# Kernel tuning notes

Measured on AMD Instinct MI355X. Metric: run time of the kernel, lower is better.

Reference implementation:

```python
import jax, jax.numpy as jnp
import numpy as np

HEADS = 16
DIM = 1024
HEAD_DIM = DIM // HEADS


def setup_inputs() -> dict:
    key = jax.random.key(0)
    k1, k2 = jax.random.split(key)
    images = jax.random.normal(k1, (2, 2048, DIM), dtype=jnp.float32)
    # torch nn.Linear(dim, 3*dim, bias=False): y = x @ W.T, W: [3*dim, dim].
    # Store as [dim, 3*dim] for direct x @ W_qkv.
    W_qkv = jax.random.normal(k2, (DIM, 3 * DIM), dtype=jnp.float32) / np.sqrt(DIM)
    return {"images": images, "W_qkv": W_qkv}


def reference(images, W_qkv):
    B, S, D = images.shape
    qkv = images @ W_qkv  # [B, S, 3D]
    q, k, v = jnp.split(qkv, 3, axis=-1)
    # [B, S, H, Dh] -> [B, H, S, Dh]
    def to_heads(t):
        return t.reshape(B, S, HEADS, HEAD_DIM).transpose(0, 2, 1, 3)
    q, k, v = to_heads(q), to_heads(k), to_heads(v)
    scale = 1.0 / jnp.sqrt(jnp.asarray(HEAD_DIM, dtype=q.dtype))
    scores = jnp.einsum('bhqd,bhkd->bhqk', q, k) * scale  # [B, H, S, S]
    probs = jax.nn.softmax(scores, axis=-1)
    out = jnp.einsum('bhqk,bhkd->bhqd', probs, v)  # [B, H, S, Dh]
    return out.transpose(0, 2, 1, 3).reshape(B, S, D)
```

## Files before the change

kernel.cpp:

```cpp
#include <hip/hip_runtime.h>
#include <hip/hip_bf16.h>
#include <math.h>

typedef __bf16 bf16x8 __attribute__((ext_vector_type(8)));
typedef float f32x4 __attribute__((ext_vector_type(4)));
typedef unsigned short u16x8 __attribute__((ext_vector_type(8)));
typedef unsigned short u16x4 __attribute__((ext_vector_type(4)));
typedef unsigned short u16;

#define S_LEN 2048
#define DMODEL 1024
#define NH 16

__device__ __forceinline__ u16 f2bf(float f) {
    __bf16 b = (__bf16)f;
    return __builtin_bit_cast(u16, b);
}
__device__ __forceinline__ float bf2f(u16 u) {
    union { unsigned int i; float f; } v; v.i = ((unsigned int)u) << 16; return v.f;
}

__device__ __forceinline__ void gload16(const u16* g, u16* lds_base) {
    __builtin_amdgcn_global_load_lds(
        (const __attribute__((address_space(1))) unsigned int*)g,
        (__attribute__((address_space(3))) unsigned int*)lds_base,
        16, 0, 0);
}

__global__ __launch_bounds__(256) void prep(const float* __restrict__ X, u16* __restrict__ Xb,
                                            const float* __restrict__ W, u16* __restrict__ Wt) {
    __shared__ u16 tile[32][33];
    const int bid = blockIdx.x;
    if (bid < 4096) {
        int i = (bid * 256 + threadIdx.x) * 4;
        float4 v = *(const float4*)(X + i);
        Xb[i + 0] = f2bf(v.x); Xb[i + 1] = f2bf(v.y);
        Xb[i + 2] = f2bf(v.z); Xb[i + 3] = f2bf(v.w);
    } else {
        int bid2 = bid - 4096;
        int n0 = (bid2 % 96) * 32, k0 = (bid2 / 96) * 32;
        int tx = threadIdx.x & 31, ty = threadIdx.x >> 5;
#pragma unroll
        for (int i = 0; i < 4; i++) {
            int k = ty + i * 8;
            tile[k][tx] = f2bf(W[(size_t)(k0 + k) * 3072 + n0 + tx]);
        }
        __syncthreads();
#pragma unroll
        for (int i = 0; i < 4; i++) {
            int n = ty + i * 8;
            Wt[(size_t)(n0 + n) * 1024 + k0 + tx] = tile[tx][n];
        }
    }
}

__global__ __launch_bounds__(256) void qkv_gemm(const u16* __restrict__ A, const u16* __restrict__ Bt,
                                                u16* __restrict__ C, u16* __restrict__ Vtp) {
    __shared__ alignas(16) u16 As[128 * 64];
    __shared__ alignas(16) u16 Bs[128 * 64];
    const int tid = threadIdx.x, l = tid & 63, w = tid >> 6;
    const int fid = blockIdx.x + blockIdx.y * 24;
    const int swz = (fid & 7) * 96 + (fid >> 3);
    const int bn = swz >> 5, bm = swz & 31;
    const int wm = w >> 1, wn = w & 1;
    const int c0 = l & 15, g = l >> 4;
    f32x4 acc[4][4] = {};
    for (int kt = 0; kt < 1024; kt += 64) {
        __syncthreads();
#pragma unroll
        for (int n = 0; n < 4; n++) {
            int i = tid + n * 256;
            int r = i >> 3, c = i & 7;
            int cs = c ^ (r & 7);
            u16* dstA = As + (size_t)(w * 64 + n * 256) * 8;
            u16* dstB = Bs + (size_t)(w * 64 + n * 256) * 8;
            gload16(A + (size_t)(bm * 128 + r) * 1024 + kt + cs * 8, dstA);
            gload16(Bt + (size_t)(bn * 128 + r) * 1024 + kt + cs * 8, dstB);
        }
        __syncthreads();
#pragma unroll
        for (int kk = 0; kk < 2; kk++) {
            bf16x8 af[4], bfr[4];
#pragma unroll
            for (int m = 0; m < 4; m++) {
                int row = wm * 64 + m * 16 + c0;
                af[m] = *(const bf16x8*)((const char*)As + row * 128 + (((g + kk * 4) ^ (row & 7)) << 4));
            }
#pragma unroll
            for (int n = 0; n < 4; n++) {
                int row = wn * 64 + n * 16 + c0;
                bfr[n] = *(const bf16x8*)((const char*)Bs + row * 128 + (((g + kk * 4) ^ (row & 7)) << 4));
            }
#pragma unroll
            for (int m = 0; m < 4; m++)
#pragma unroll
                for (int n = 0; n < 4; n++)
                    acc[m][n] = __builtin_amdgcn_mfma_f32_16x16x32_bf16(af[m], bfr[n], acc[m][n], 0, 0, 0);
        }
    }
    if (bn < 16) {
#pragma unroll
        for (int m = 0; m < 4; m++)
#pragma unroll
            for (int n = 0; n < 4; n++)
#pragma unroll
                for (int j = 0; j < 4; j++) {
                    int row = bm * 128 + wm * 64 + m * 16 + 4 * g + j;
                    int col = bn * 128 + wn * 64 + n * 16 + c0;
                    C[(size_t)row * 3072 + col] = f2bf(acc[m][n][j]);
                }
    } else {
        const int h = (bn - 16) * 2 + wn;
#pragma unroll
        for (int m = 0; m < 4; m++) {
            int srow_g = bm * 128 + wm * 64 + m * 16 + 4 * g;
            int b = srow_g >> 11;
            int srow = srow_g & 2047;
            int sbase = (srow & ~63) + 32 * (m >> 1) + 8 * g + 4 * (m & 1);
#pragma unroll
            for (int n = 0; n < 4; n++) {
                int d = n * 16 + c0;
                u16x4 v;
#pragma unroll
                for (int j = 0; j < 4; j++) v[j] = f2bf(acc[m][n][j]);
                *(u16x4*)(Vtp + ((size_t)(b * 16 + h) * 64 + d) * S_LEN + sbase) = v;
            }
        }
    }
}

__global__ __launch_bounds__(512, 4) void attn11(const u16* __restrict__ QKV, const u16* __restrict__ Vtp,
                                                 float* __restrict__ outp) {
    __shared__ alignas(16) u16 Ks[2][2][64 * 64];
    __shared__ alignas(16) u16 Vs[2][2][64 * 64];
    const int bid = blockIdx.x;
    const int wg = ((bid & 7) << 7) | (bid >> 3);
    const int tid = threadIdx.x, l = tid & 63, w = tid >> 6;
    const int hf = w >> 2, wsub = w & 3;
    const int qt = wg & 31, bh = wg >> 5;
    const int b = bh >> 4, h = bh & 15;
    const int c0 = l & 15, g = l >> 4;
    const u16* Qb = QKV + (size_t)b * S_LEN * 3072 + h * 64;
    const u16* Kb = Qb + 1024;
    const u16* Vb = Vtp + (size_t)bh * 64 * S_LEN;
    const int kv0 = hf * 1024;
    const int qrow = qt * 64 + wsub * 16 + c0;

    const int tid_h = tid & 255;
    const int r0 = tid_h >> 3, cs0 = (tid_h & 7) ^ (r0 & 7);
    const int i1 = tid_h + 256, r1 = i1 >> 3, cs1 = (i1 & 7) ^ (r1 & 7);
    const int dbA = (wsub * 64) * 8, dbB = (256 + wsub * 64) * 8;

    int off[8];
#pragma unroll
    for (int x = 0; x < 4; x++)
#pragma unroll
        for (int kk = 0; kk < 2; kk++)
            off[x * 2 + kk] = (x * 16 + c0) * 128 + (((g + 4 * kk) ^ (c0 & 7)) << 4);

    bf16x8 qf[2];
    {
        const float qs = 0.125f * 1.44269504f;
#pragma unroll
        for (int kk = 0; kk < 2; kk++) {
            u16x8 v = *(const u16x8*)(Qb + (size_t)qrow * 3072 + kk * 32 + g * 8);
            bf16x8 q;
#pragma unroll
            for (int j = 0; j < 8; j++) q[j] = (__bf16)(bf2f(v[j]) * qs);
            qf[kk] = q;
        }
    }
    bf16x8 vone;
#pragma unroll
    for (int j = 0; j < 8; j++) vone[j] = (__bf16)1.0f;

    float m_r = 0.f;
    f32x4 accO[4] = {};
    f32x4 accL = {};

    gload16(Kb + (size_t)(kv0 + r0) * 3072 + cs0 * 8, Ks[hf][0] + dbA);
    gload16(Kb + (size_t)(kv0 + r1) * 3072 + cs1 * 8, Ks[hf][0] + dbB);
    gload16(Vb + (size_t)r0 * S_LEN + kv0 + cs0 * 8, Vs[hf][0] + dbA);
    gload16(Vb + (size_t)r1 * S_LEN + kv0 + cs1 * 8, Vs[hf][0] + dbB);

    for (int t = 0; t < 16; t++) {
        const int cur = t & 1;
        __syncthreads();
        if (t + 1 < 16) {
            const int kvn = kv0 + (t + 1) * 64;
            gload16(Kb + (size_t)(kvn + r0) * 3072 + cs0 * 8, Ks[hf][cur ^ 1] + dbA);
            gload16(Kb + (size_t)(kvn + r1) * 3072 + cs1 * 8, Ks[hf][cur ^ 1] + dbB);
            gload16(Vb + (size_t)r0 * S_LEN + kvn + cs0 * 8, Vs[hf][cur ^ 1] + dbA);
            gload16(Vb + (size_t)r1 * S_LEN + kvn + cs1 * 8, Vs[hf][cur ^ 1] + dbB);
        }
        const char* Kc = (const char*)Ks[hf][cur];
        const char* Vc = (const char*)Vs[hf][cur];
        f32x4 sc[4];
        const float nm = -m_r;
#pragma unroll
        for (int kb = 0; kb < 4; kb++) { sc[kb][0] = nm; sc[kb][1] = nm; sc[kb][2] = nm; sc[kb][3] = nm; }
        __builtin_amdgcn_s_setprio(1);
#pragma unroll
        for (int kb = 0; kb < 4; kb++)
#pragma unroll
            for (int kk = 0; kk < 2; kk++) {
                bf16x8 kf = *(const bf16x8*)(Kc + off[kb * 2 + kk]);
                sc[kb] = __builtin_amdgcn_mfma_f32_16x16x32_bf16(kf, qf[kk], sc[kb], 0, 0, 0);
            }
        __builtin_amdgcn_s_setprio(0);
        bf16x8 vf[2][4];
#pragma unroll
        for (int kk = 0; kk < 2; kk++)
#pragma unroll
            for (int n = 0; n < 4; n++)
                vf[kk][n] = *(const bf16x8*)(Vc + off[n * 2 + kk]);
        float m0 = fmaxf(fmaxf(sc[0][0], sc[0][1]), sc[0][2]);
        float m1 = fmaxf(fmaxf(sc[0][3], sc[1][0]), sc[1][1]);
        float m2 = fmaxf(fmaxf(sc[1][2], sc[1][3]), sc[2][0]);
        float m3 = fmaxf(fmaxf(sc[2][1], sc[2][2]), sc[2][3]);
        float m4 = fmaxf(fmaxf(sc[3][0], sc[3][1]), sc[3][2]);
        float mx = fmaxf(fmaxf(fmaxf(m0, m1), m2), fmaxf(fmaxf(m3, m4), sc[3][3]));
        if (!__all(mx <= 8.f)) {
            float mxr = fmaxf(mx, __shfl_xor(mx, 16));
            mxr = fmaxf(mxr, __shfl_xor(mxr, 32));
            float adj = fmaxf(mxr, 0.f);
            float alpha = __builtin_amdgcn_exp2f(-adj);
            m_r += adj;
#pragma unroll
            for (int j = 0; j < 4; j++) {
                float aj = __shfl(alpha, 20 * g + j);
                accL[j] *= aj;
#pragma unroll
                for (int n = 0; n < 4; n++) accO[n][j] *= aj;
            }
#pragma unroll
            for (int kb = 0; kb < 4; kb++)
#pragma unroll
                for (int j = 0; j < 4; j++) sc[kb][j] -= adj;
        }
#pragma unroll
        for (int kb = 0; kb < 4; kb++)
#pragma unroll
            for (int j = 0; j < 4; j++)
                sc[kb][j] = __builtin_amdgcn_exp2f(sc[kb][j]);
        __builtin_amdgcn_s_setprio(1);
#pragma unroll
        for (int kk = 0; kk < 2; kk++) {
            bf16x8 pf;
#pragma unroll
            for (int j = 0; j < 4; j++) {
                pf[j]     = (__bf16)sc[2 * kk][j];
                pf[j + 4] = (__bf16)sc[2 * kk + 1][j];
            }
            accL = __builtin_amdgcn_mfma_f32_16x16x32_bf16(pf, vone, accL, 0, 0, 0);
#pragma unroll
            for (int n = 0; n < 4; n++)
                accO[n] = __builtin_amdgcn_mfma_f32_16x16x32_bf16(pf, vf[kk][n], accO[n], 0, 0, 0);
        }
        __builtin_amdgcn_s_setprio(0);
    }
    __syncthreads();
    float* Opart = (float*)&Ks[0][0][0];
    float* m1s   = (float*)&Vs[0][0][0];
    float* l1s   = m1s + 64;
    if (hf == 1) {
#pragma unroll
        for (int j = 0; j < 4; j++) {
            int rj = wsub * 16 + 4 * g + j;
#pragma unroll
            for (int n = 0; n < 4; n++) Opart[rj * 65 + n * 16 + c0] = accO[n][j];
        }
        if (g == 0) m1s[wsub * 16 + c0] = m_r;
        if (c0 == 0) {
#pragma unroll
            for (int j = 0; j < 4; j++) l1s[wsub * 16 + 4 * g + j] = accL[j];
        }
    }
    __syncthreads();
    if (hf == 0) {
#pragma unroll
        for (int j = 0; j < 4; j++) {
            int rj = wsub * 16 + 4 * g + j;
            float m1v = m1s[rj], l1v = l1s[rj];
            float m0v = __shfl(m_r, 20 * g + j);
            float M = fmaxf(m0v, m1v);
            float a0 = __builtin_amdgcn_exp2f(m0v - M);
            float a1 = __builtin_amdgcn_exp2f(m1v - M);
            float inv = 1.0f / (a0 * accL[j] + a1 * l1v);
            float* op = outp + ((size_t)b * S_LEN + qt * 64 + rj) * DMODEL + h * 64;
#pragma unroll
            for (int n = 0; n < 4; n++)
                op[n * 16 + c0] = (a0 * accO[n][j] + a1 * Opart[rj * 65 + n * 16 + c0]) * inv;
        }
    }
}

extern "C" void kernel_launch(void* const* d_in, const int* in_sizes, int n_in,
                              void* d_out, int out_size, void* d_ws, size_t ws_size,
                              hipStream_t stream) {
    const float* X = (const float*)d_in[0];
    const float* W = (const float*)d_in[1];
    float* out = (float*)d_out;

    u16* Xb  = (u16*)d_ws;
    u16* Wt  = Xb + (size_t)4096 * 1024;
    u16* QKV = Wt + (size_t)3072 * 1024;
    u16* Vtp = QKV + (size_t)4096 * 3072;

    prep<<<7168, 256, 0, stream>>>(X, Xb, W, Wt);
    qkv_gemm<<<dim3(24, 32), 256, 0, stream>>>(Xb, Wt, QKV, Vtp);
    attn11<<<1024, 512, 0, stream>>>(QKV, Vtp, out);
}
```

Baseline: 103.3 us.

## Double-buffer QKV GEMM LDS tiles with prefetch and MFMA priority

Restructures the QKV projection GEMM main loop to use two LDS buffers with a K-tile of 32 instead of one 64-wide tile. It issues async global-to-LDS loads for the next tile before computing the current one, which removes one barrier per iteration. It also changes the XOR swizzle for the narrower rows, precomputes LDS read offsets, and raises wave priority around the MFMA block. The cost is twice as many loop iterations with smaller tiles per barrier, and the overlap depends on when the compiler's wait for the async loads lands relative to the barrier.

```diff
diff --git a/kernel.cpp b/kernel.cpp
--- a/kernel.cpp
+++ b/kernel.cpp
@@ -56,47 +56,61 @@
 
 __global__ __launch_bounds__(256) void qkv_gemm(const u16* __restrict__ A, const u16* __restrict__ Bt,
                                                 u16* __restrict__ C, u16* __restrict__ Vtp) {
-    __shared__ alignas(16) u16 As[128 * 64];
-    __shared__ alignas(16) u16 Bs[128 * 64];
+    __shared__ alignas(16) u16 As[2][128 * 32];
+    __shared__ alignas(16) u16 Bs[2][128 * 32];
     const int tid = threadIdx.x, l = tid & 63, w = tid >> 6;
     const int fid = blockIdx.x + blockIdx.y * 24;
     const int swz = (fid & 7) * 96 + (fid >> 3);
     const int bn = swz >> 5, bm = swz & 31;
     const int wm = w >> 1, wn = w & 1;
     const int c0 = l & 15, g = l >> 4;
+
+    const int r0 = tid >> 2, c0s = (tid & 3) ^ ((r0 >> 1) & 3);
+    const int i1 = tid + 256, r1 = i1 >> 2, c1s = (i1 & 3) ^ ((r1 >> 1) & 3);
+    const int db0 = (w * 64) * 8, db1 = (256 + w * 64) * 8;
+
+    int aoff[4], boff[4];
+#pragma unroll
+    for (int m = 0; m < 4; m++) {
+        int row = wm * 64 + m * 16 + c0;
+        aoff[m] = row * 64 + ((g ^ ((row >> 1) & 3)) << 4);
+    }
+#pragma unroll
+    for (int n = 0; n < 4; n++) {
+        int row = wn * 64 + n * 16 + c0;
+        boff[n] = row * 64 + ((g ^ ((row >> 1) & 3)) << 4);
+    }
+
     f32x4 acc[4][4] = {};
-    for (int kt = 0; kt < 1024; kt += 64) {
+    gload16(A + (size_t)(bm * 128 + r0) * 1024 + c0s * 8, As[0] + db0);
+    gload16(A + (size_t)(bm * 128 + r1) * 1024 + c1s * 8, As[0] + db1);
+    gload16(Bt + (size_t)(bn * 128 + r0) * 1024 + c0s * 8, Bs[0] + db0);
+    gload16(Bt + (size_t)(bn * 128 + r1) * 1024 + c1s * 8, Bs[0] + db1);
+
+    for (int t = 0; t < 32; t++) {
+        const int cur = t & 1;
         __syncthreads();
-#pragma unroll
-        for (int n = 0; n < 4; n++) {
-            int i = tid + n * 256;
-            int r = i >> 3, c = i & 7;
-            int cs = c ^ (r & 7);
-            u16* dstA = As + (size_t)(w * 64 + n * 256) * 8;
-            u16* dstB = Bs + (size_t)(w * 64 + n * 256) * 8;
-            gload16(A + (size_t)(bm * 128 + r) * 1024 + kt + cs * 8, dstA);
-            gload16(Bt + (size_t)(bn * 128 + r) * 1024 + kt + cs * 8, dstB);
-        }
-        __syncthreads();
-#pragma unroll
-        for (int kk = 0; kk < 2; kk++) {
-            bf16x8 af[4], bfr[4];
-#pragma unroll
-            for (int m = 0; m < 4; m++) {
-                int row = wm * 64 + m * 16 + c0;
-                af[m] = *(const bf16x8*)((const char*)As + row * 128 + (((g + kk * 4) ^ (row & 7)) << 4));
-            }
-#pragma unroll
-            for (int n = 0; n < 4; n++) {
-                int row = wn * 64 + n * 16 + c0;
-                bfr[n] = *(const bf16x8*)((const char*)Bs + row * 128 + (((g + kk * 4) ^ (row & 7)) << 4));
-            }
-#pragma unroll
-            for (int m = 0; m < 4; m++)
-#pragma unroll
-                for (int n = 0; n < 4; n++)
-                    acc[m][n] = __builtin_amdgcn_mfma_f32_16x16x32_bf16(af[m], bfr[n], acc[m][n], 0, 0, 0);
-        }
+        if (t + 1 < 32) {
+            const int kt = (t + 1) * 32;
+            gload16(A + (size_t)(bm * 128 + r0) * 1024 + kt + c0s * 8, As[cur ^ 1] + db0);
+            gload16(A + (size_t)(bm * 128 + r1) * 1024 + kt + c1s * 8, As[cur ^ 1] + db1);
+            gload16(Bt + (size_t)(bn * 128 + r0) * 1024 + kt + c0s * 8, Bs[cur ^ 1] + db0);
+            gload16(Bt + (size_t)(bn * 128 + r1) * 1024 + kt + c1s * 8, Bs[cur ^ 1] + db1);
+        }
+        const char* Ac = (const char*)As[cur];
+        const char* Bc = (const char*)Bs[cur];
+        bf16x8 af[4], bfr[4];
+#pragma unroll
+        for (int m = 0; m < 4; m++) af[m] = *(const bf16x8*)(Ac + aoff[m]);
+#pragma unroll
+        for (int n = 0; n < 4; n++) bfr[n] = *(const bf16x8*)(Bc + boff[n]);
+        __builtin_amdgcn_s_setprio(1);
+#pragma unroll
+        for (int m = 0; m < 4; m++)
+#pragma unroll
+            for (int n = 0; n < 4; n++)
+                acc[m][n] = __builtin_amdgcn_mfma_f32_16x16x32_bf16(af[m], bfr[n], acc[m][n], 0, 0, 0);
+        __builtin_amdgcn_s_setprio(0);
     }
     if (bn < 16) {
 #pragma unroll
```

Result: faster. 98.52 us (-4.7%).
